# Kernel optimization log

Hardware: AMD Instinct MI355X
Metric: run time of the kernel (lower is better)

Reference implementation:

```python
import jax, jax.numpy as jnp
import numpy as np

NUM_CLASSES = 80
CONF_THRE = 0.2
NMS_THRE = 0.45
MAX_DET = 300   # fixed cap replacing torch's variable-length NMS output (padded + keep mask)
IMG = 640.0


def setup_inputs() -> dict:
    key = jax.random.key(0)
    k1, k2 = jax.random.split(key)
    pred = jax.random.uniform(k1, (32, 8400, 85), dtype=jnp.float32)
    # scale cx,cy,w,h to pixel range so IoU/NMS geometry is realistic
    pred = pred.at[..., :4].multiply(IMG)
    zone = jax.random.uniform(k2, (8, 2), dtype=jnp.float32) * IMG
    return {"prediction": pred, "zone": zone}


def _pairwise_iou(b):
    # b: [B, K, 4] in x1y1x2y2
    area = jnp.clip(b[..., 2] - b[..., 0], 0.0) * jnp.clip(b[..., 3] - b[..., 1], 0.0)
    lt = jnp.maximum(b[:, :, None, :2], b[:, None, :, :2])
    rb = jnp.minimum(b[:, :, None, 2:], b[:, None, :, 2:])
    wh = jnp.clip(rb - lt, 0.0)
    inter = wh[..., 0] * wh[..., 1]
    return inter / (area[:, :, None] + area[:, None, :] - inter + 1e-9)


def _postprocess(prediction):
    # decode cx,cy,w,h -> x1,y1,x2,y2
    xy = prediction[..., :2]
    wh = prediction[..., 2:4]
    boxes = jnp.concatenate([xy - wh * 0.5, xy + wh * 0.5], axis=-1)  # [B,N,4]
    obj = prediction[..., 4]                                           # [B,N]
    cls = prediction[..., 5:5 + NUM_CLASSES]
    class_conf = jnp.max(cls, axis=-1)                                 # [B,N]
    class_pred = jnp.argmax(cls, axis=-1)                              # [B,N]

    # confidence mask (obj * class_conf >= thre); invalid -> -inf so top_k drops them
    nms_score = obj * class_conf
    nms_score = jnp.where(nms_score >= CONF_THRE, nms_score, -jnp.inf)

    s, idx = jax.lax.top_k(nms_score, MAX_DET)                         # [B,K]
    b = jnp.take_along_axis(boxes, idx[..., None], axis=1)             # [B,K,4]

    # class-agnostic greedy NMS on score-sorted boxes (matches torchvision.ops.nms)
    iou = _pairwise_iou(b)                                             # [B,K,K]
    keep = jnp.isfinite(s)                                             # valid (passed conf) entries
    ar = jnp.arange(MAX_DET)
    def body(i, keep):
        sup = keep[:, i][:, None] & (iou[:, i, :] > NMS_THRE) & (ar > i)
        return keep & jnp.logical_not(sup)
    keep = jax.lax.fori_loop(0, MAX_DET, body, keep)

    obj_s = jnp.take_along_axis(obj, idx, axis=1)
    conf_s = jnp.take_along_axis(class_conf, idx, axis=1)
    cls_s = jnp.take_along_axis(class_pred, idx, axis=1).astype(jnp.int32)
    # extract_boxes_scores_and_classes: score = max over columns [obj, class_conf]
    scores = jnp.maximum(obj_s, conf_s)
    return b, scores, cls_s, keep


def _points_inside_zone(px, py, zone):
    # px, py: [B,K]; zone: [Z,2]. Ray-casting parity test (faithful to torch version).
    zr = jnp.roll(zone, shift=1, axis=0)
    xi, yi = zone[:, 0], zone[:, 1]
    xj, yj = zr[:, 0], zr[:, 1]
    pyb = py[..., None]  # [B,K,1] vs [Z]
    pxb = px[..., None]
    gyi = yi > pyb
    gyj = yj > pyb
    gx = (xj - xi) * (pyb - yi) / (yj - yi) + xi
    inter = (gyi != gyj) & (gx > pxb)
    return (jnp.sum(inter.astype(jnp.int32), axis=-1) % 2) > 0


def reference(prediction, zone):
    b, scores, classes, keep = _postprocess(prediction)
    cx = (b[..., 0] + b[..., 2]) * 0.5
    cy = (b[..., 1] + b[..., 3]) * 0.5
    in_zone = _points_inside_zone(cx, cy, zone) & keep
    centers_yx = jnp.stack([cy, cx], axis=-1)                          # [B,K,2]
    boxes_yxyx = jnp.stack([b[..., 1], b[..., 0], b[..., 3], b[..., 2]], axis=-1)
    return boxes_yxyx, in_zone, scores, classes, centers_yx, keep
```

## Files before the change

### kernel.cpp

```cpp
#include <hip/hip_runtime.h>
#include <stdint.h>

typedef unsigned long long ull;

#define NA 8400
#define NB 32
#define KTOP 300
#define NC 80
#define TB 512
#define CH 17
#define NBIN 309
#define HSTR 311
#define NCPY 8
#define BASEK 0xBE4CCCCDu
#define CANDMAX 512

#define O1 38400
#define O2 48000
#define O3 57600
#define O4 67200
#define O5 86400

__global__ __launch_bounds__(256) void score_kernel(const float* __restrict__ pred,
                                                    uint32_t* __restrict__ keys) {
    __shared__ float sP[128 * 85];
    const int blk = blockIdx.x;
    const float4* g4 = (const float4*)(pred + (size_t)blk * 128 * 85);
    float4* l4 = (float4*)sP;
    for (int i = threadIdx.x; i < (128 * 85 / 4); i += 256) l4[i] = g4[i];
    __syncthreads();
    const int t = threadIdx.x;
    if (t < 128) {
        const float* p = sP + t * 85;
        float obj = p[4];
        float b0 = p[5], b1 = p[6], b2 = p[7], b3 = p[8];
        #pragma unroll
        for (int c = 4; c < NC; c += 4) {
            b0 = fmaxf(b0, p[5 + c]);
            b1 = fmaxf(b1, p[6 + c]);
            b2 = fmaxf(b2, p[7 + c]);
            b3 = fmaxf(b3, p[8 + c]);
        }
        float best = fmaxf(fmaxf(b0, b1), fmaxf(b2, b3));
        float sc = obj * best;
        uint32_t u = (sc >= 0.2f) ? (__float_as_uint(sc) | 0x80000000u) : 0x007FFFFFu;
        keys[(size_t)blk * 128 + t] = u;
    }
}

__device__ __forceinline__ uint32_t key_bin(uint32_t k) {
    return (k < BASEK) ? 0u : (1u + ((k - BASEK) >> 16));
}

__global__ __launch_bounds__(TB) void batch_kernel(const float* __restrict__ pred,
                                                   const float* __restrict__ zone,
                                                   const uint32_t* __restrict__ keys,
                                                   float* __restrict__ out) {
    #pragma clang fp contract(off)
    __shared__ uint32_t sH[NCPY * HSTR];
    __shared__ ull sSel[KTOP];
    __shared__ ull sSorted[KTOP];
    __shared__ ull sCand[CANDMAX];
    __shared__ float sB0[KTOP], sB1[KTOP], sB2[KTOP], sB3[KTOP];
    __shared__ ull sMask[KTOP * 5];
    __shared__ uint32_t sWTot[8];
    __shared__ uint32_t sBc[2];
    __shared__ uint32_t sPar[KTOP];
    __shared__ ull sKeepF[5];
    __shared__ float sZone[16];
    __shared__ uint32_t sCN;

    const int b = blockIdx.x;
    const int t = threadIdx.x;
    const int lane = t & 63;
    const int wv = t >> 6;

    uint32_t myk[CH];
    #pragma unroll
    for (int e = 0; e < CH; ++e) {
        int idx = e * TB + t;
        myk[e] = (idx < NA) ? keys[(size_t)b * NA + idx] : 0u;
    }
    for (int i = t; i < NCPY * HSTR; i += TB) sH[i] = 0u;
    if (t < 16) sZone[t] = zone[t];
    __syncthreads();

    {
        uint32_t* hw = &sH[wv * HSTR];
        #pragma unroll
        for (int e = 0; e < CH; ++e)
            atomicAdd(&hw[key_bin(myk[e])], 1u);
    }
    __syncthreads();

    uint32_t v = 0, s = 0;
    if (t < 320) {
        if (t < NBIN) {
            #pragma unroll
            for (int c = 0; c < NCPY; ++c) v += sH[c * HSTR + t];
        }
        s = v;
        #pragma unroll
        for (int off = 1; off < 64; off <<= 1) {
            uint32_t o = __shfl_down(s, off, 64);
            if (lane + off < 64) s += o;
        }
        if (lane == 0) sWTot[wv] = s;
    }
    __syncthreads();
    if (t < 320) {
        uint32_t S = s;
        for (int w2 = wv + 1; w2 < 5; ++w2) S += sWTot[w2];
        uint32_t above = S - v;
        if (above < KTOP && S >= KTOP) {
            sBc[0] = (uint32_t)t;
            sBc[1] = KTOP - above;
        }
    }
    __syncthreads();
    const uint32_t Tbin = sBc[0];
    const uint32_t rem = sBc[1];
    const uint32_t cntgt = KTOP - rem;

    {
        uint32_t gtc = 0, eqc = 0;
        #pragma unroll
        for (int e = 0; e < CH; ++e) {
            uint32_t bin = key_bin(myk[e]);
            gtc += (bin > Tbin) ? 1u : 0u;
            eqc += (bin == Tbin) ? 1u : 0u;
        }
        uint32_t pack = (gtc << 16) | eqc;
        uint32_t ps = pack;
        #pragma unroll
        for (int off = 1; off < 64; off <<= 1) {
            uint32_t o = __shfl_up(ps, off, 64);
            if (lane >= off) ps += o;
        }
        if (lane == 63) sWTot[wv] = ps;
        __syncthreads();
        uint32_t excl = ps - pack;
        #pragma unroll
        for (int w2 = 0; w2 < 8; ++w2) if (w2 < wv) excl += sWTot[w2];
        uint32_t gtoff = excl >> 16;
        uint32_t eqoff = excl & 0xFFFFu;
        if (t == TB - 1) {
            uint32_t tot = eqoff + eqc;
            sCN = (tot > CANDMAX) ? CANDMAX : tot;
        }
        #pragma unroll
        for (int e = 0; e < CH; ++e) {
            uint32_t k = myk[e];
            uint32_t bin = key_bin(k);
            uint32_t idx = (uint32_t)(e * TB + t);
            if (bin > Tbin) {
                sSel[gtoff++] = ((ull)k << 32) | (ull)(0xFFFFFFFFu - idx);
            } else if (bin == Tbin) {
                if (eqoff < CANDMAX)
                    sCand[eqoff] = ((ull)k << 32) | (ull)(0xFFFFFFFFu - idx);
                eqoff++;
            }
        }
        __syncthreads();
    }

    {
        int cn = (int)sCN;
        if (t < cn) {
            ull my = sCand[t];
            uint32_t rk = 0;
            for (int j = 0; j < cn; ++j) rk += (sCand[j] > my) ? 1u : 0u;
            if (rk < rem) sSel[cntgt + rk] = my;
        }
        __syncthreads();
    }

    const size_t bo = (size_t)b * KTOP;
    for (int tt = t; tt < 2 * KTOP; tt += TB) {
        const int row = tt >> 1;
        const int half = tt & 1;
        const ull selv = sSel[row];
        const uint32_t a = 0xFFFFFFFFu - (uint32_t)selv;
        const float* p = pred + ((size_t)b * NA + a) * 85;
        const int cbase = half * 40;
        float v0 = p[5 + cbase], v1 = p[6 + cbase], v2 = p[7 + cbase], v3 = p[8 + cbase];
        int   c0 = cbase, c1 = cbase + 1, c2 = cbase + 2, c3 = cbase + 3;
        #pragma unroll
        for (int c = 4; c < 40; c += 4) {
            float w0 = p[5 + cbase + c],     w1 = p[6 + cbase + c];
            float w2 = p[7 + cbase + c],     w3 = p[8 + cbase + c];
            if (w0 > v0) { v0 = w0; c0 = cbase + c; }
            if (w1 > v1) { v1 = w1; c1 = cbase + c + 1; }
            if (w2 > v2) { v2 = w2; c2 = cbase + c + 2; }
            if (w3 > v3) { v3 = w3; c3 = cbase + c + 3; }
        }
        uint32_t rk = 0;
        const int jb = half * 150;
        for (int j = jb; j < jb + 150; ++j)
            rk += (sSel[j] > selv) ? 1u : 0u;
        float bv = v0; int bc = c0;
        if (v1 > bv || (v1 == bv && c1 < bc)) { bv = v1; bc = c1; }
        if (v2 > bv || (v2 == bv && c2 < bc)) { bv = v2; bc = c2; }
        if (v3 > bv || (v3 == bv && c3 < bc)) { bv = v3; bc = c3; }
        float pv = __shfl_xor(bv, 1, 64);
        int   pc = __shfl_xor(bc, 1, 64);
        uint32_t rko = __shfl_xor(rk, 1, 64);
        const uint32_t rank = rk + rko;
        if (half == 0) {
            if (pv > bv) { bv = pv; bc = pc; }
            float x = p[0], y = p[1], w = p[2], h = p[3], obj = p[4];
            float hw = w * 0.5f, hh = h * 0.5f;
            float x1 = x - hw, y1 = y - hh, x2 = x + hw, y2 = y + hh;
            sSorted[rank] = selv;
            sB0[rank] = x1; sB1[rank] = y1; sB2[rank] = x2; sB3[rank] = y2;
            out[(bo + rank) * 4 + 0] = y1;
            out[(bo + rank) * 4 + 1] = x1;
            out[(bo + rank) * 4 + 2] = y2;
            out[(bo + rank) * 4 + 3] = x2;
            out[O4 + (bo + rank) * 2 + 0] = (y1 + y2) * 0.5f;
            out[O4 + (bo + rank) * 2 + 1] = (x1 + x2) * 0.5f;
            out[O2 + bo + rank] = fmaxf(obj, bv);
            out[O3 + bo + rank] = (float)bc;
        }
    }
    __syncthreads();

    for (int p2 = t; p2 < KTOP * 5; p2 += TB) {
        const int role = p2 / KTOP;
        const int i = p2 - role * KTOP;
        const int j0 = role * 64;
        int jmax = j0 + 64; if (jmax > KTOP) jmax = KTOP;
        if (jmax <= i + 1) { sMask[i * 5 + role] = 0ull; continue; }
        float x1 = sB0[i], y1 = sB1[i], x2 = sB2[i], y2 = sB3[i];
        float ai = fmaxf(x2 - x1, 0.0f) * fmaxf(y2 - y1, 0.0f);
        ull bits = 0ull;
        for (int j = j0; j < jmax; ++j) {
            float bx1 = sB0[j], by1 = sB1[j], bx2 = sB2[j], by2 = sB3[j];
            float aj = fmaxf(bx2 - bx1, 0.0f) * fmaxf(by2 - by1, 0.0f);
            float iw = fminf(x2, bx2) - fmaxf(x1, bx1); iw = fmaxf(iw, 0.0f);
            float ih = fminf(y2, by2) - fmaxf(y1, by1); ih = fmaxf(ih, 0.0f);
            float inter = iw * ih;
            float den = ai + aj;
            den = den - inter;
            den = den + 1e-9f;
            float iou = inter / den;
            if (j > i && iou > 0.45f) bits |= (1ull << (j - j0));
        }
        sMask[i * 5 + role] = bits;
    }
    __syncthreads();

    if (wv == 0) {
        ull rm[5][5];
        ull kw[5];
        #pragma unroll
        for (int w = 0; w < 5; ++w) {
            int i = w * 64 + lane;
            bool f = (i < KTOP) && (((uint32_t)(sSorted[i] >> 32)) > 0x007FFFFFu);
            kw[w] = __ballot(f);
            #pragma unroll
            for (int ww = 0; ww < 5; ++ww)
                rm[w][ww] = (i < KTOP) ? sMask[i * 5 + ww] : 0ull;
        }
        #pragma unroll
        for (int w = 0; w < 5; ++w) {
            ull cur = kw[w];
            while (cur) {
                int ib = __builtin_ctzll(cur);
                ull m0 = __shfl(rm[w][0], ib);
                ull m1 = __shfl(rm[w][1], ib);
                ull m2 = __shfl(rm[w][2], ib);
                ull m3 = __shfl(rm[w][3], ib);
                ull m4 = __shfl(rm[w][4], ib);
                kw[0] &= ~m0; kw[1] &= ~m1; kw[2] &= ~m2; kw[3] &= ~m3; kw[4] &= ~m4;
                ull done = (ib == 63) ? 0ull : (~0ull << (ib + 1));
                cur = kw[w] & done;
            }
        }
        if (lane == 0) {
            #pragma unroll
            for (int w = 0; w < 5; ++w) sKeepF[w] = kw[w];
        }
    } else if (t >= 64 && t < 64 + KTOP) {
        const int i = t - 64;
        float cy = (sB1[i] + sB3[i]) * 0.5f;
        float cx = (sB0[i] + sB2[i]) * 0.5f;
        int cnt = 0;
        #pragma unroll
        for (int e = 0; e < 8; ++e) {
            float xi = sZone[2 * e], yi = sZone[2 * e + 1];
            int ep = (e + 7) & 7;
            float xj = sZone[2 * ep], yj = sZone[2 * ep + 1];
            bool gyi = yi > cy, gyj = yj > cy;
            if (gyi != gyj) {
                float gx = (xj - xi) * (cy - yi) / (yj - yi) + xi;
                if (gx > cx) cnt++;
            }
        }
        sPar[i] = (uint32_t)(cnt & 1);
    }
    __syncthreads();

    if (t < KTOP) {
        int kp = (int)((sKeepF[t >> 6] >> (t & 63)) & 1ull);
        int inz = (sPar[t] && kp) ? 1 : 0;
        out[O1 + bo + t] = (float)inz;
        out[O5 + bo + t] = (float)kp;
    }
}

extern "C" void kernel_launch(void* const* d_in, const int* in_sizes, int n_in,
                              void* d_out, int out_size, void* d_ws, size_t ws_size,
                              hipStream_t stream) {
    const float* pred = (const float*)d_in[0];
    const float* zone = (const float*)d_in[1];
    float* out = (float*)d_out;
    uint32_t* keys = (uint32_t*)d_ws;

    score_kernel<<<(NB * NA) / 128, 256, 0, stream>>>(pred, keys);
    batch_kernel<<<NB, TB, 0, stream>>>(pred, zone, keys, out);
}
```

Measured before the change: 185.7 us.

## Register-tile IoU mask over 4 rows, pack boxes as float4, ballot zero-bin histogram

Each thread in the IoU mask stage now computes four rows against one shared column box, loading it once as a float4 with a precomputed area, which cuts LDS traffic and redundant area math. The zero-bin histogram increments, the most common case, are replaced by a wave ballot and popcount with a single atomic per wave, reducing LDS atomic contention. The rank count reads sSel as 128-bit pairs, and launch bounds request two blocks per CU. In exchange, only 375 threads work in the mask stage, and the occupancy hint may raise register pressure.

```diff
diff --git a/kernel.cpp b/kernel.cpp
--- a/kernel.cpp
+++ b/kernel.cpp
@@ -52,16 +52,17 @@
     return (k < BASEK) ? 0u : (1u + ((k - BASEK) >> 16));
 }
 
-__global__ __launch_bounds__(TB) void batch_kernel(const float* __restrict__ pred,
-                                                   const float* __restrict__ zone,
-                                                   const uint32_t* __restrict__ keys,
-                                                   float* __restrict__ out) {
+__global__ __launch_bounds__(TB, 2) void batch_kernel(const float* __restrict__ pred,
+                                                      const float* __restrict__ zone,
+                                                      const uint32_t* __restrict__ keys,
+                                                      float* __restrict__ out) {
     #pragma clang fp contract(off)
     __shared__ uint32_t sH[NCPY * HSTR];
-    __shared__ ull sSel[KTOP];
+    __shared__ __align__(16) ull sSel[KTOP];
     __shared__ ull sSorted[KTOP];
     __shared__ ull sCand[CANDMAX];
-    __shared__ float sB0[KTOP], sB1[KTOP], sB2[KTOP], sB3[KTOP];
+    __shared__ float4 sBox[KTOP];
+    __shared__ float sA[KTOP];
     __shared__ ull sMask[KTOP * 5];
     __shared__ uint32_t sWTot[8];
     __shared__ uint32_t sBc[2];
@@ -87,9 +88,16 @@
 
     {
         uint32_t* hw = &sH[wv * HSTR];
-        #pragma unroll
-        for (int e = 0; e < CH; ++e)
-            atomicAdd(&hw[key_bin(myk[e])], 1u);
+        uint32_t c0 = 0;
+        #pragma unroll
+        for (int e = 0; e < CH; ++e) {
+            uint32_t k = myk[e];
+            ull m = __ballot(k < BASEK);
+            c0 += (uint32_t)__popcll(m);
+            if (k >= BASEK)
+                atomicAdd(&hw[1u + ((k - BASEK) >> 16)], 1u);
+        }
+        if (lane == 0) atomicAdd(&hw[0], c0);
     }
     __syncthreads();
 
@@ -176,6 +184,7 @@
     }
 
     const size_t bo = (size_t)b * KTOP;
+    const ulonglong2* sSel2 = (const ulonglong2*)sSel;
     for (int tt = t; tt < 2 * KTOP; tt += TB) {
         const int row = tt >> 1;
         const int half = tt & 1;
@@ -195,9 +204,12 @@
             if (w3 > v3) { v3 = w3; c3 = cbase + c + 3; }
         }
         uint32_t rk = 0;
-        const int jb = half * 150;
-        for (int j = jb; j < jb + 150; ++j)
-            rk += (sSel[j] > selv) ? 1u : 0u;
+        const int pb = half * 75;
+        for (int jp = pb; jp < pb + 75; ++jp) {
+            ulonglong2 vv = sSel2[jp];
+            rk += (vv.x > selv) ? 1u : 0u;
+            rk += (vv.y > selv) ? 1u : 0u;
+        }
         float bv = v0; int bc = c0;
         if (v1 > bv || (v1 == bv && c1 < bc)) { bv = v1; bc = c1; }
         if (v2 > bv || (v2 == bv && c2 < bc)) { bv = v2; bc = c2; }
@@ -212,7 +224,8 @@
             float hw = w * 0.5f, hh = h * 0.5f;
             float x1 = x - hw, y1 = y - hh, x2 = x + hw, y2 = y + hh;
             sSorted[rank] = selv;
-            sB0[rank] = x1; sB1[rank] = y1; sB2[rank] = x2; sB3[rank] = y2;
+            sBox[rank] = make_float4(x1, y1, x2, y2);
+            sA[rank] = fmaxf(x2 - x1, 0.0f) * fmaxf(y2 - y1, 0.0f);
             out[(bo + rank) * 4 + 0] = y1;
             out[(bo + rank) * 4 + 1] = x1;
             out[(bo + rank) * 4 + 2] = y2;
@@ -225,28 +238,54 @@
     }
     __syncthreads();
 
-    for (int p2 = t; p2 < KTOP * 5; p2 += TB) {
-        const int role = p2 / KTOP;
-        const int i = p2 - role * KTOP;
+    if (t < 375) {
+        const int role = t / 75;
+        const int i0 = (t - role * 75) * 4;
         const int j0 = role * 64;
         int jmax = j0 + 64; if (jmax > KTOP) jmax = KTOP;
-        if (jmax <= i + 1) { sMask[i * 5 + role] = 0ull; continue; }
-        float x1 = sB0[i], y1 = sB1[i], x2 = sB2[i], y2 = sB3[i];
-        float ai = fmaxf(x2 - x1, 0.0f) * fmaxf(y2 - y1, 0.0f);
-        ull bits = 0ull;
-        for (int j = j0; j < jmax; ++j) {
-            float bx1 = sB0[j], by1 = sB1[j], bx2 = sB2[j], by2 = sB3[j];
-            float aj = fmaxf(bx2 - bx1, 0.0f) * fmaxf(by2 - by1, 0.0f);
-            float iw = fminf(x2, bx2) - fmaxf(x1, bx1); iw = fmaxf(iw, 0.0f);
-            float ih = fminf(y2, by2) - fmaxf(y1, by1); ih = fmaxf(ih, 0.0f);
-            float inter = iw * ih;
-            float den = ai + aj;
-            den = den - inter;
-            den = den + 1e-9f;
-            float iou = inter / den;
-            if (j > i && iou > 0.45f) bits |= (1ull << (j - j0));
-        }
-        sMask[i * 5 + role] = bits;
+        float4 bi0 = sBox[i0],     bi1 = sBox[i0 + 1];
+        float4 bi2 = sBox[i0 + 2], bi3 = sBox[i0 + 3];
+        float a0 = sA[i0], a1 = sA[i0 + 1], a2 = sA[i0 + 2], a3 = sA[i0 + 3];
+        ull bits0 = 0ull, bits1 = 0ull, bits2 = 0ull, bits3 = 0ull;
+        if (jmax > i0 + 1) {
+            for (int j = j0; j < jmax; ++j) {
+                float4 bj = sBox[j];
+                float aj = sA[j];
+                ull bit = 1ull << (j - j0);
+                {
+                    float iw = fminf(bi0.z, bj.z) - fmaxf(bi0.x, bj.x); iw = fmaxf(iw, 0.0f);
+                    float ih = fminf(bi0.w, bj.w) - fmaxf(bi0.y, bj.y); ih = fmaxf(ih, 0.0f);
+                    float inter = iw * ih;
+                    float den = a0 + aj; den = den - inter; den = den + 1e-9f;
+                    if (j > i0 && inter / den > 0.45f) bits0 |= bit;
+                }
+                {
+                    float iw = fminf(bi1.z, bj.z) - fmaxf(bi1.x, bj.x); iw = fmaxf(iw, 0.0f);
+                    float ih = fminf(bi1.w, bj.w) - fmaxf(bi1.y, bj.y); ih = fmaxf(ih, 0.0f);
+                    float inter = iw * ih;
+                    float den = a1 + aj; den = den - inter; den = den + 1e-9f;
+                    if (j > i0 + 1 && inter / den > 0.45f) bits1 |= bit;
+                }
+                {
+                    float iw = fminf(bi2.z, bj.z) - fmaxf(bi2.x, bj.x); iw = fmaxf(iw, 0.0f);
+                    float ih = fminf(bi2.w, bj.w) - fmaxf(bi2.y, bj.y); ih = fmaxf(ih, 0.0f);
+                    float inter = iw * ih;
+                    float den = a2 + aj; den = den - inter; den = den + 1e-9f;
+                    if (j > i0 + 2 && inter / den > 0.45f) bits2 |= bit;
+                }
+                {
+                    float iw = fminf(bi3.z, bj.z) - fmaxf(bi3.x, bj.x); iw = fmaxf(iw, 0.0f);
+                    float ih = fminf(bi3.w, bj.w) - fmaxf(bi3.y, bj.y); ih = fmaxf(ih, 0.0f);
+                    float inter = iw * ih;
+                    float den = a3 + aj; den = den - inter; den = den + 1e-9f;
+                    if (j > i0 + 3 && inter / den > 0.45f) bits3 |= bit;
+                }
+            }
+        }
+        sMask[(i0 + 0) * 5 + role] = bits0;
+        sMask[(i0 + 1) * 5 + role] = bits1;
+        sMask[(i0 + 2) * 5 + role] = bits2;
+        sMask[(i0 + 3) * 5 + role] = bits3;
     }
     __syncthreads();
 
@@ -283,8 +322,9 @@
         }
     } else if (t >= 64 && t < 64 + KTOP) {
         const int i = t - 64;
-        float cy = (sB1[i] + sB3[i]) * 0.5f;
-        float cx = (sB0[i] + sB2[i]) * 0.5f;
+        float4 bi = sBox[i];
+        float cy = (bi.y + bi.w) * 0.5f;
+        float cx = (bi.x + bi.z) * 0.5f;
         int cnt = 0;
         #pragma unroll
         for (int e = 0; e < 8; ++e) {
```

Result: slower. 227.1 us (+22.3%).
